# Kernel tuning notes

Measured on AMD Instinct MI355X. Metric: run time of the kernel, lower is better.

The kernel has to match this reference:

```python
import jax, jax.numpy as jnp
import numpy as np

DIM = 1024          # hidden_size
MOE_HID = 512       # moe_intermediate_size
SHARED_HID = 2048   # shared_expert_intermediate_size
N_EXPERTS = 16
TOP_K = 2
NORM_TOPK_PROB = True


def setup_inputs() -> dict:
    key = jax.random.key(0)
    ks = jax.random.split(key, 9)
    s = 0.02  # init scale
    x = jax.random.normal(ks[0], (2, 1024, DIM), dtype=jnp.float32)
    Wg = jax.random.normal(ks[1], (N_EXPERTS, DIM), dtype=jnp.float32) * s
    We_gate = jax.random.normal(ks[2], (N_EXPERTS, MOE_HID, DIM), dtype=jnp.float32) * s
    We_up = jax.random.normal(ks[3], (N_EXPERTS, MOE_HID, DIM), dtype=jnp.float32) * s
    We_down = jax.random.normal(ks[4], (N_EXPERTS, DIM, MOE_HID), dtype=jnp.float32) * s
    Ws_gate = jax.random.normal(ks[5], (SHARED_HID, DIM), dtype=jnp.float32) * s
    Ws_up = jax.random.normal(ks[6], (SHARED_HID, DIM), dtype=jnp.float32) * s
    Ws_down = jax.random.normal(ks[7], (DIM, SHARED_HID), dtype=jnp.float32) * s
    Wsg = jax.random.normal(ks[8], (1, DIM), dtype=jnp.float32) * s
    return {"x": x, "Wg": Wg, "We_gate": We_gate, "We_up": We_up,
            "We_down": We_down, "Ws_gate": Ws_gate, "Ws_up": Ws_up,
            "Ws_down": Ws_down, "Wsg": Wsg}


def reference(x, Wg, We_gate, We_up, We_down, Ws_gate, Ws_up, Ws_down, Wsg):
    B, S, D = x.shape
    xt = x.reshape(-1, D)  # [T, D] tokens
    # router: softmax over experts, then top-k
    gates = jax.nn.softmax(xt @ Wg.T, axis=-1)          # [T, E]
    scores, inds = jax.lax.top_k(gates, TOP_K)           # [T, K]
    if NORM_TOPK_PROB:
        scores = scores / jnp.sum(scores, axis=-1, keepdims=True)
    # experts: SwiGLU computed for all experts, then gather the top-k outputs
    g = jnp.einsum('td,ehd->teh', xt, We_gate)           # [T, E, H]
    u = jnp.einsum('td,ehd->teh', xt, We_up)             # [T, E, H]
    h = jax.nn.silu(g) * u                               # swiglu
    y_all = jnp.einsum('teh,edh->ted', h, We_down)       # [T, E, D]
    y_sel = jnp.take_along_axis(y_all, inds[:, :, None], axis=1)  # [T, K, D]
    y = jnp.sum(y_sel * scores[:, :, None], axis=1)      # [T, D]
    # shared expert with sigmoid gate
    shared = (jax.nn.silu(xt @ Ws_gate.T) * (xt @ Ws_up.T)) @ Ws_down.T  # [T, D]
    y = y + jax.nn.sigmoid(xt @ Wsg.T) * shared
    return y.reshape(B, S, D)
```

## Files before the change

kernel.cpp:

```cpp
#include <hip/hip_runtime.h>
#include <stdint.h>

#define DIM 1024
#define MOE_HID 512
#define SH_HID 2048
#define NE 16
#define NT 2048
#define ROWS_CAP 6144

typedef unsigned short u16;
typedef __attribute__((ext_vector_type(8))) short s16x8;
typedef __attribute__((ext_vector_type(4))) float f32x4;

#define SYNC_BAR() \
  asm volatile("s_waitcnt lgkmcnt(0)" ::: "memory"); \
  __builtin_amdgcn_sched_barrier(0); \
  __builtin_amdgcn_s_barrier(); \
  __builtin_amdgcn_sched_barrier(0);

__device__ __forceinline__ u16 f2bf(float f){
  union { float f; unsigned v; } x; x.f = f;
  unsigned r = x.v + 0x7FFF + ((x.v >> 16) & 1);
  return (u16)(r >> 16);
}

__device__ __forceinline__ s16x8 cvt8pk(float4 a, float4 b){
  union { s16x8 v; unsigned u[4]; } r;
  asm volatile("v_cvt_pk_bf16_f32 %0, %1, %2" : "=v"(r.u[0]) : "v"(a.x), "v"(a.y));
  asm volatile("v_cvt_pk_bf16_f32 %0, %1, %2" : "=v"(r.u[1]) : "v"(a.z), "v"(a.w));
  asm volatile("v_cvt_pk_bf16_f32 %0, %1, %2" : "=v"(r.u[2]) : "v"(b.x), "v"(b.y));
  asm volatile("v_cvt_pk_bf16_f32 %0, %1, %2" : "=v"(r.u[3]) : "v"(b.z), "v"(b.w));
  return r.v;
}

__global__ void k_cvt_x(const float* __restrict__ s, u16* __restrict__ d){
  int i = (blockIdx.x * 256 + threadIdx.x) * 4;
  float4 v = *(const float4*)(s + i);
  ushort4 o;
  o.x = f2bf(v.x); o.y = f2bf(v.y); o.z = f2bf(v.z); o.w = f2bf(v.w);
  *(ushort4*)(d + i) = o;
}

__global__ void k_router(const float* __restrict__ x, const float* __restrict__ Wg,
                         const float* __restrict__ Wsgate1,
                         int* __restrict__ inds, float* __restrict__ scores,
                         float* __restrict__ gl){
  int lane = threadIdx.x & 63;
  int t = blockIdx.x * 4 + (threadIdx.x >> 6);
  const float4* xt = (const float4*)(x + (size_t)t * DIM);
  float4 xv[4];
#pragma unroll
  for(int j = 0; j < 4; j++) xv[j] = xt[lane + 64 * j];

  float acc[NE + 1];
#pragma unroll
  for(int e = 0; e <= NE; e++) acc[e] = 0.f;

#pragma unroll
  for(int e = 0; e < NE; e++){
    const float4* wr = (const float4*)(Wg + (size_t)e * DIM);
#pragma unroll
    for(int j = 0; j < 4; j++){
      float4 w = wr[lane + 64 * j];
      acc[e] += xv[j].x * w.x + xv[j].y * w.y + xv[j].z * w.z + xv[j].w * w.w;
    }
  }
  {
    const float4* wr = (const float4*)Wsgate1;
#pragma unroll
    for(int j = 0; j < 4; j++){
      float4 w = wr[lane + 64 * j];
      acc[NE] += xv[j].x * w.x + xv[j].y * w.y + xv[j].z * w.z + xv[j].w * w.w;
    }
  }

#pragma unroll
  for(int off = 32; off; off >>= 1)
#pragma unroll
    for(int e = 0; e <= NE; e++) acc[e] += __shfl_xor(acc[e], off, 64);

  if(lane == 0){
    int b0 = 0; float v0 = acc[0];
    for(int e = 1; e < NE; e++) if(acc[e] > v0){ v0 = acc[e]; b0 = e; }
    int b1 = (b0 == 0) ? 1 : 0; float v1 = acc[b1];
    for(int e = 0; e < NE; e++) if(e != b0 && acc[e] > v1){ v1 = acc[e]; b1 = e; }
    float s0 = 1.f / (1.f + __expf(v1 - v0));
    inds[t*2+0] = b0; inds[t*2+1] = b1;
    scores[t*2+0] = s0; scores[t*2+1] = 1.f - s0;
    gl[t] = acc[NE];
  }
}

__global__ void k_assign(const int* __restrict__ inds, const float* __restrict__ scores,
                         int* __restrict__ counts, int* __restrict__ offs,
                         int* __restrict__ rowinfo, float* __restrict__ rowscore){
  __shared__ int cnt[NE], off_s[NE], fill[NE];
  int tid = threadIdx.x;
  if(tid < NE){ cnt[tid] = 0; fill[tid] = 0; }
  __syncthreads();
  int ea[4];
#pragma unroll
  for(int i = 0; i < 4; i++){
    int a = tid + 1024 * i;
    ea[i] = inds[a];
    atomicAdd(&cnt[ea[i]], 1);
  }
  __syncthreads();
  if(tid == 0){
    int o = 0;
    for(int e = 0; e < NE; e++){
      off_s[e] = o;
      o += (cnt[e] + 127) & ~127;
    }
  }
  __syncthreads();
#pragma unroll
  for(int i = 0; i < 4; i++){
    int a = tid + 1024 * i;
    int e = ea[i];
    int row = off_s[e] + atomicAdd(&fill[e], 1);
    rowinfo[row] = a;
    rowscore[row] = scores[a];
  }
  if(tid < NE){ counts[tid] = cnt[tid]; offs[tid] = off_s[tid]; }
}

__global__ __launch_bounds__(256, 2) void k_gateup_fused(
    const u16* __restrict__ xb, const int* __restrict__ rowinfo,
    const float* __restrict__ Weg, const float* __restrict__ Weu,
    const float* __restrict__ Wsg, const float* __restrict__ Wsu,
    u16* __restrict__ Hm, u16* __restrict__ Hs,
    const int* __restrict__ counts, const int* __restrict__ offs){
  __shared__ __align__(16) u16 As[2][128 * 64];
  __shared__ __align__(16) u16 Bgs[2][64 * 64];
  __shared__ __align__(16) u16 Bus[2][64 * 64];

  const int bid = blockIdx.x;
  const int tid = threadIdx.x, lane = tid & 63, wid = tid >> 6;
  const int wm = wid >> 1, wn = wid & 1;
  const int srow = tid >> 2;
  const int p16 = (tid & 3) * 16;
  const int cb = (tid & 3) * 2;
  const int key = srow & 7;
  const int fr = lane & 15;
  const int fc = lane >> 4;
  const int fx = fr & 7;

  const int wA00 = (srow     ) * 64 + ((cb    ) ^ key) * 8;
  const int wA01 = (srow     ) * 64 + ((cb + 1) ^ key) * 8;
  const int wA10 = (srow + 64) * 64 + ((cb    ) ^ key) * 8;
  const int wA11 = (srow + 64) * 64 + ((cb + 1) ^ key) * 8;
  const int wB0  = srow * 64 + ((cb    ) ^ key) * 8;
  const int wB1  = srow * 64 + ((cb + 1) ^ key) * 8;

  const u16 *Ar0, *Ar1;
  const float *Bgr, *Bur;
  u16* H; int ldh;

  if(bid < 384){
    const int row0 = (bid >> 3) * 128;
    const int n0 = (bid & 7) * 64;
    const int rows_used = offs[NE-1] + ((counts[NE-1] + 127) & ~127);
    if(row0 >= rows_used) return;
    int e = 0;
#pragma unroll
    for(int k = 1; k < NE; k++) if(row0 >= offs[k]) e = k;

    int a0 = rowinfo[row0 + srow];
    int a1 = rowinfo[row0 + 64 + srow];
    int t0 = ((unsigned)a0 < 4096u) ? (a0 >> 1) : 0;
    int t1 = ((unsigned)a1 < 4096u) ? (a1 >> 1) : 0;
    Ar0 = xb + (size_t)t0 * DIM + p16;
    Ar1 = xb + (size_t)t1 * DIM + p16;
    Bgr = Weg + (size_t)e * MOE_HID * DIM + (size_t)((bid & 7) * 64 + srow) * DIM + p16;
    Bur = Weu + (size_t)e * MOE_HID * DIM + (size_t)((bid & 7) * 64 + srow) * DIM + p16;
    H = Hm + (size_t)row0 * MOE_HID + n0;
    ldh = MOE_HID;
  } else {
    const int i = bid - 384;
    const int row0 = (i >> 5) * 128;
    const int n0 = (i & 31) * 64;
    Ar0 = xb + (size_t)(row0 + srow) * DIM + p16;
    Ar1 = xb + (size_t)(row0 + 64 + srow) * DIM + p16;
    Bgr = Wsg + (size_t)(n0 + srow) * DIM + p16;
    Bur = Wsu + (size_t)(n0 + srow) * DIM + p16;
    H = Hs + (size_t)row0 * SH_HID + n0;
    ldh = SH_HID;
  }

  uint4 aE00, aE01, aE10, aE11, aO00, aO01, aO10, aO11;
  float4 gE0, gE1, gE2, gE3, uE0, uE1, uE2, uE3;
  float4 gO0, gO1, gO2, gO3, uO0, uO1, uO2, uO3;

#define GF_LOAD(S, ko) \
  a##S##00 = *(const uint4*)(Ar0 + (ko));      a##S##01 = *(const uint4*)(Ar0 + (ko) + 8); \
  a##S##10 = *(const uint4*)(Ar1 + (ko));      a##S##11 = *(const uint4*)(Ar1 + (ko) + 8); \
  g##S##0 = *(const float4*)(Bgr + (ko));      g##S##1 = *(const float4*)(Bgr + (ko) + 4); \
  g##S##2 = *(const float4*)(Bgr + (ko) + 8);  g##S##3 = *(const float4*)(Bgr + (ko) + 12); \
  u##S##0 = *(const float4*)(Bur + (ko));      u##S##1 = *(const float4*)(Bur + (ko) + 4); \
  u##S##2 = *(const float4*)(Bur + (ko) + 8);  u##S##3 = *(const float4*)(Bur + (ko) + 12);

  f32x4 accg[4][2], accu[4][2];
#pragma unroll
  for(int m = 0; m < 4; m++)
#pragma unroll
    for(int n = 0; n < 2; n++){
      accg[m][n] = (f32x4){0.f,0.f,0.f,0.f};
      accu[m][n] = (f32x4){0.f,0.f,0.f,0.f};
    }

  GF_LOAD(E, 0)
  GF_LOAD(O, 64)

#define GF_STEP(tt, S, bb) { \
  *(uint4*)(As[bb] + wA00) = a##S##00; \
  *(uint4*)(As[bb] + wA01) = a##S##01; \
  *(uint4*)(As[bb] + wA10) = a##S##10; \
  *(uint4*)(As[bb] + wA11) = a##S##11; \
  *(s16x8*)(Bgs[bb] + wB0) = cvt8pk(g##S##0, g##S##1); \
  *(s16x8*)(Bgs[bb] + wB1) = cvt8pk(g##S##2, g##S##3); \
  *(s16x8*)(Bus[bb] + wB0) = cvt8pk(u##S##0, u##S##1); \
  *(s16x8*)(Bus[bb] + wB1) = cvt8pk(u##S##2, u##S##3); \
  SYNC_BAR() \
  if((tt) + 2 < 16){ GF_LOAD(S, ((tt) + 2) * 64) } \
  s16x8 af[4][2], bgf[2][2], buf2[2][2]; \
  _Pragma("unroll") for(int m = 0; m < 4; m++){ \
    int r = wm*64 + m*16 + fr; \
    _Pragma("unroll") for(int ks = 0; ks < 2; ks++) \
      af[m][ks] = *(const s16x8*)(As[bb] + r*64 + (((ks*4 + fc) ^ fx)) * 8); } \
  _Pragma("unroll") for(int n = 0; n < 2; n++){ \
    int r = wn*32 + n*16 + fr; \
    _Pragma("unroll") for(int ks = 0; ks < 2; ks++){ \
      bgf[n][ks]  = *(const s16x8*)(Bgs[bb] + r*64 + (((ks*4 + fc) ^ fx)) * 8); \
      buf2[n][ks] = *(const s16x8*)(Bus[bb] + r*64 + (((ks*4 + fc) ^ fx)) * 8); } } \
  _Pragma("unroll") for(int m = 0; m < 4; m++) \
  _Pragma("unroll") for(int n = 0; n < 2; n++){ \
    accg[m][n] = __builtin_amdgcn_mfma_f32_16x16x32_bf16(af[m][0], bgf[n][0], accg[m][n], 0, 0, 0); \
    accg[m][n] = __builtin_amdgcn_mfma_f32_16x16x32_bf16(af[m][1], bgf[n][1], accg[m][n], 0, 0, 0); \
    accu[m][n] = __builtin_amdgcn_mfma_f32_16x16x32_bf16(af[m][0], buf2[n][0], accu[m][n], 0, 0, 0); \
    accu[m][n] = __builtin_amdgcn_mfma_f32_16x16x32_bf16(af[m][1], buf2[n][1], accu[m][n], 0, 0, 0); } }

  for(int t = 0; t < 16; t += 2){
    GF_STEP(t,     E, 0)
    GF_STEP(t + 1, O, 1)
  }

#pragma unroll
  for(int m = 0; m < 4; m++)
#pragma unroll
    for(int n = 0; n < 2; n++)
#pragma unroll
      for(int i = 0; i < 4; i++){
        int r = wm*64 + m*16 + ((lane >> 4) << 2) + i;
        int c = wn*32 + n*16 + (lane & 15);
        float g = accg[m][n][i], u = accu[m][n][i];
        float h = (g / (1.f + __expf(-g))) * u;
        H[(size_t)r * ldh + c] = f2bf(h);
      }
}

__global__ __launch_bounds__(256, 2) void k_down_all(
    const u16* __restrict__ Hm, const u16* __restrict__ Hs,
    const float* __restrict__ Wed, const float* __restrict__ Wsd,
    float* __restrict__ yp, float* __restrict__ Sh0, float* __restrict__ Sh1,
    const int* __restrict__ counts, const int* __restrict__ offs,
    const int* __restrict__ rowinfo, const float* __restrict__ rowscore){
  __shared__ __align__(16) u16 As[2][128 * 32];
  __shared__ __align__(16) u16 Bs[2][128 * 32];

  const int y = blockIdx.y, n0 = blockIdx.x * 128;
  const bool sh = (y < 32);
  const u16* A; const float* B; float* O = yp;
  int lda, M = NT, row0 = 0, kBeg = 0, nk, lrow = 0;
  if(sh){
    int mtile = y & 15, kz = y >> 4;
    A = Hs + (size_t)mtile * 128 * SH_HID; lda = SH_HID;
    B = Wsd; kBeg = kz * 1024; nk = 32;
    O = (kz == 0) ? Sh0 : Sh1;
    row0 = mtile * 128;
  } else {
    row0 = (y - 32) * 128;
    int rows_used = offs[NE-1] + ((counts[NE-1] + 127) & ~127);
    if(row0 >= rows_used) return;
    int e = 0;
#pragma unroll
    for(int k = 1; k < NE; k++) if(row0 >= offs[k]) e = k;
    M = counts[e];
    lrow = row0 - offs[e];
    A = Hm + (size_t)row0 * MOE_HID; lda = MOE_HID;
    B = Wed + (size_t)e * DIM * MOE_HID; nk = 16;
  }

  const int tid = threadIdx.x, lane = tid & 63, wid = tid >> 6;
  const int wm = wid >> 1, wn = wid & 1;
  const int srow = tid >> 2, p8 = (tid & 3) * 8;
  const int swz8 = (((tid & 3) ^ ((tid >> 3) & 3))) * 8;
  const int fr = lane & 15;
  const int fkswz = (((lane >> 4) ^ ((lane >> 1) & 3))) * 8;
  const int wA0 = srow * 32 + swz8, wA1 = (64 + srow) * 32 + swz8;

  const u16* Ar0 = A + (size_t)srow * lda + kBeg + p8;
  const u16* Ar1 = A + (size_t)(64 + srow) * lda + kBeg + p8;
  const float* Br0 = B + (size_t)(n0 + srow) * lda + kBeg + p8;
  const float* Br1 = B + (size_t)(n0 + 64 + srow) * lda + kBeg + p8;

  uint4 aE0, aE1, aO0, aO1;
  float4 bE00, bE01, bE10, bE11, bO00, bO01, bO10, bO11;

#define DN_LOAD(S, ko) \
  a##S##0 = *(const uint4*)(Ar0 + (ko));   a##S##1 = *(const uint4*)(Ar1 + (ko)); \
  b##S##00 = *(const float4*)(Br0 + (ko)); b##S##01 = *(const float4*)(Br0 + (ko) + 4); \
  b##S##10 = *(const float4*)(Br1 + (ko)); b##S##11 = *(const float4*)(Br1 + (ko) + 4);

  f32x4 acc[4][4];
#pragma unroll
  for(int m = 0; m < 4; m++)
#pragma unroll
    for(int n = 0; n < 4; n++) acc[m][n] = (f32x4){0.f,0.f,0.f,0.f};

  DN_LOAD(E, 0)
  DN_LOAD(O, 32)

#define DN_STEP(tt, S, bb) { \
  *(uint4*)(As[bb] + wA0) = a##S##0; \
  *(uint4*)(As[bb] + wA1) = a##S##1; \
  *(s16x8*)(Bs[bb] + wA0) = cvt8pk(b##S##00, b##S##01); \
  *(s16x8*)(Bs[bb] + wA1) = cvt8pk(b##S##10, b##S##11); \
  SYNC_BAR() \
  if((tt) + 2 < nk){ DN_LOAD(S, ((tt) + 2) * 32) } \
  s16x8 af[4], bf[4]; \
  _Pragma("unroll") for(int m = 0; m < 4; m++) \
    af[m] = *(const s16x8*)(As[bb] + (wm*64 + m*16 + fr) * 32 + fkswz); \
  _Pragma("unroll") for(int n = 0; n < 4; n++) \
    bf[n] = *(const s16x8*)(Bs[bb] + (wn*64 + n*16 + fr) * 32 + fkswz); \
  _Pragma("unroll") for(int m = 0; m < 4; m++) \
  _Pragma("unroll") for(int n = 0; n < 4; n++) \
    acc[m][n] = __builtin_amdgcn_mfma_f32_16x16x32_bf16(af[m], bf[n], acc[m][n], 0, 0, 0); }

  for(int t = 0; t < nk; t += 2){
    DN_STEP(t,     E, 0)
    DN_STEP(t + 1, O, 1)
  }

#pragma unroll
  for(int m = 0; m < 4; m++)
#pragma unroll
    for(int i = 0; i < 4; i++){
      int rl = wm*64 + m*16 + ((lane >> 4) << 2) + i;
      if(sh){
        float* orow = O + (size_t)(row0 + rl) * DIM + n0 + wn*64 + (lane & 15);
#pragma unroll
        for(int n = 0; n < 4; n++) orow[n*16] = acc[m][n][i];
      } else if(lrow + rl < M){
        int ar = row0 + rl;
        int slot = rowinfo[ar];
        float sc = rowscore[ar];
        float* orow = yp + (size_t)slot * DIM + n0 + wn*64 + (lane & 15);
#pragma unroll
        for(int n = 0; n < 4; n++) orow[n*16] = sc * acc[m][n][i];
      }
    }
}

__global__ void k_combine(const float* __restrict__ yp, const float* __restrict__ Sh0,
                          const float* __restrict__ Sh1,
                          const float* __restrict__ gl, float* __restrict__ out){
  int idx = (blockIdx.x * 256 + threadIdx.x) * 4;
  int t = idx >> 10;
  float s = 1.f / (1.f + __expf(-gl[t]));
  float4 a = *(const float4*)(yp + (size_t)(t*2)   * DIM + (idx & 1023));
  float4 b = *(const float4*)(yp + (size_t)(t*2+1) * DIM + (idx & 1023));
  float4 c0 = *(const float4*)(Sh0 + idx);
  float4 c1 = *(const float4*)(Sh1 + idx);
  float4 o;
  o.x = a.x + b.x + s * (c0.x + c1.x);
  o.y = a.y + b.y + s * (c0.y + c1.y);
  o.z = a.z + b.z + s * (c0.z + c1.z);
  o.w = a.w + b.w + s * (c0.w + c1.w);
  *(float4*)(out + idx) = o;
}

extern "C" void kernel_launch(void* const* d_in, const int* in_sizes, int n_in,
                              void* d_out, int out_size, void* d_ws, size_t ws_size,
                              hipStream_t stream){
  const float* x    = (const float*)d_in[0];
  const float* Wg   = (const float*)d_in[1];
  const float* Weg  = (const float*)d_in[2];
  const float* Weu  = (const float*)d_in[3];
  const float* Wed  = (const float*)d_in[4];
  const float* Wsg  = (const float*)d_in[5];
  const float* Wsu  = (const float*)d_in[6];
  const float* Wsd  = (const float*)d_in[7];
  const float* Wg1  = (const float*)d_in[8];
  float* out = (float*)d_out;

  char* p = (char*)d_ws;
  int* inds   = (int*)p;  p += 4096 * 4;
  float* scores = (float*)p; p += 4096 * 4;
  float* gl   = (float*)p;  p += NT * 4;
  int* counts = (int*)p;  p += 64;
  int* offs   = (int*)p;  p += 64;
  int* rowinfo = (int*)p; p += ROWS_CAP * 4;
  float* rowscore = (float*)p; p += ROWS_CAP * 4;
  u16* xb     = (u16*)p;  p += (size_t)NT * DIM * 2;
  u16* Hs     = (u16*)p;  p += (size_t)NT * SH_HID * 2;
  float* Sh0  = (float*)p; p += (size_t)NT * DIM * 4;
  float* Sh1  = (float*)p; p += (size_t)NT * DIM * 4;
  u16* Hm     = (u16*)p;  p += (size_t)ROWS_CAP * MOE_HID * 2;
  float* yp   = (float*)p; p += (size_t)NT * 2 * DIM * 4;

  k_router<<<NT/4, 256, 0, stream>>>(x, Wg, Wg1, inds, scores, gl);
  k_cvt_x<<<NT * DIM / (256 * 4), 256, 0, stream>>>(x, xb);
  k_assign<<<1, 1024, 0, stream>>>(inds, scores, counts, offs, rowinfo, rowscore);

  k_gateup_fused<<<896, 256, 0, stream>>>(xb, rowinfo, Weg, Weu, Wsg, Wsu,
                                          Hm, Hs, counts, offs);
  k_down_all<<<dim3(8, 80), 256, 0, stream>>>(Hm, Hs, Wed, Wsd,
                                              yp, Sh0, Sh1, counts, offs,
                                              rowinfo, rowscore);

  k_combine<<<2048, 256, 0, stream>>>(yp, Sh0, Sh1, gl, out);
}
```

Before: 115.6 us.

## Fuse x bf16 conversion into router and combine via atomic adds in down kernel

The fp32-to-bf16 conversion of x moves into the router kernel, which already loads x, so one launch and one extra read of x go away. The separate combine kernel and its intermediate buffers (yp, Sh0, Sh1) are removed. The down-projection kernel now scales by the sigmoid shared gate or the routing score and atomically adds straight into a zero-initialised output. This drops several large fp32 intermediate writes and reads, at the cost of a memset, fp32 atomic traffic, and a summation order that is no longer deterministic.

```diff
diff --git a/kernel.cpp b/kernel.cpp
--- a/kernel.cpp
+++ b/kernel.cpp
@@ -33,24 +33,23 @@
   return r.v;
 }
 
-__global__ void k_cvt_x(const float* __restrict__ s, u16* __restrict__ d){
-  int i = (blockIdx.x * 256 + threadIdx.x) * 4;
-  float4 v = *(const float4*)(s + i);
-  ushort4 o;
-  o.x = f2bf(v.x); o.y = f2bf(v.y); o.z = f2bf(v.z); o.w = f2bf(v.w);
-  *(ushort4*)(d + i) = o;
-}
-
 __global__ void k_router(const float* __restrict__ x, const float* __restrict__ Wg,
                          const float* __restrict__ Wsgate1,
                          int* __restrict__ inds, float* __restrict__ scores,
-                         float* __restrict__ gl){
+                         float* __restrict__ gl, u16* __restrict__ xb){
   int lane = threadIdx.x & 63;
   int t = blockIdx.x * 4 + (threadIdx.x >> 6);
   const float4* xt = (const float4*)(x + (size_t)t * DIM);
   float4 xv[4];
 #pragma unroll
   for(int j = 0; j < 4; j++) xv[j] = xt[lane + 64 * j];
+
+#pragma unroll
+  for(int j = 0; j < 4; j++){
+    ushort4 o;
+    o.x = f2bf(xv[j].x); o.y = f2bf(xv[j].y); o.z = f2bf(xv[j].z); o.w = f2bf(xv[j].w);
+    *(ushort4*)(xb + (size_t)t * DIM + 4 * (lane + 64 * j)) = o;
+  }
 
   float acc[NE + 1];
 #pragma unroll
@@ -262,7 +261,7 @@
 __global__ __launch_bounds__(256, 2) void k_down_all(
     const u16* __restrict__ Hm, const u16* __restrict__ Hs,
     const float* __restrict__ Wed, const float* __restrict__ Wsd,
-    float* __restrict__ yp, float* __restrict__ Sh0, float* __restrict__ Sh1,
+    float* __restrict__ out, const float* __restrict__ gl,
     const int* __restrict__ counts, const int* __restrict__ offs,
     const int* __restrict__ rowinfo, const float* __restrict__ rowscore){
   __shared__ __align__(16) u16 As[2][128 * 32];
@@ -270,13 +269,12 @@
 
   const int y = blockIdx.y, n0 = blockIdx.x * 128;
   const bool sh = (y < 32);
-  const u16* A; const float* B; float* O = yp;
+  const u16* A; const float* B;
   int lda, M = NT, row0 = 0, kBeg = 0, nk, lrow = 0;
   if(sh){
     int mtile = y & 15, kz = y >> 4;
     A = Hs + (size_t)mtile * 128 * SH_HID; lda = SH_HID;
     B = Wsd; kBeg = kz * 1024; nk = 32;
-    O = (kz == 0) ? Sh0 : Sh1;
     row0 = mtile * 128;
   } else {
     row0 = (y - 32) * 128;
@@ -348,36 +346,21 @@
     for(int i = 0; i < 4; i++){
       int rl = wm*64 + m*16 + ((lane >> 4) << 2) + i;
       if(sh){
-        float* orow = O + (size_t)(row0 + rl) * DIM + n0 + wn*64 + (lane & 15);
-#pragma unroll
-        for(int n = 0; n < 4; n++) orow[n*16] = acc[m][n][i];
+        int token = row0 + rl;
+        float s = 1.f / (1.f + __expf(-gl[token]));
+        float* orow = out + (size_t)token * DIM + n0 + wn*64 + (lane & 15);
+#pragma unroll
+        for(int n = 0; n < 4; n++) atomicAdd(&orow[n*16], s * acc[m][n][i]);
       } else if(lrow + rl < M){
         int ar = row0 + rl;
         int slot = rowinfo[ar];
         float sc = rowscore[ar];
-        float* orow = yp + (size_t)slot * DIM + n0 + wn*64 + (lane & 15);
-#pragma unroll
-        for(int n = 0; n < 4; n++) orow[n*16] = sc * acc[m][n][i];
+        int token = slot >> 1;
+        float* orow = out + (size_t)token * DIM + n0 + wn*64 + (lane & 15);
+#pragma unroll
+        for(int n = 0; n < 4; n++) atomicAdd(&orow[n*16], sc * acc[m][n][i]);
       }
     }
-}
-
-__global__ void k_combine(const float* __restrict__ yp, const float* __restrict__ Sh0,
-                          const float* __restrict__ Sh1,
-                          const float* __restrict__ gl, float* __restrict__ out){
-  int idx = (blockIdx.x * 256 + threadIdx.x) * 4;
-  int t = idx >> 10;
-  float s = 1.f / (1.f + __expf(-gl[t]));
-  float4 a = *(const float4*)(yp + (size_t)(t*2)   * DIM + (idx & 1023));
-  float4 b = *(const float4*)(yp + (size_t)(t*2+1) * DIM + (idx & 1023));
-  float4 c0 = *(const float4*)(Sh0 + idx);
-  float4 c1 = *(const float4*)(Sh1 + idx);
-  float4 o;
-  o.x = a.x + b.x + s * (c0.x + c1.x);
-  o.y = a.y + b.y + s * (c0.y + c1.y);
-  o.z = a.z + b.z + s * (c0.z + c1.z);
-  o.w = a.w + b.w + s * (c0.w + c1.w);
-  *(float4*)(out + idx) = o;
 }
 
 extern "C" void kernel_launch(void* const* d_in, const int* in_sizes, int n_in,
@@ -404,20 +387,16 @@
   float* rowscore = (float*)p; p += ROWS_CAP * 4;
   u16* xb     = (u16*)p;  p += (size_t)NT * DIM * 2;
   u16* Hs     = (u16*)p;  p += (size_t)NT * SH_HID * 2;
-  float* Sh0  = (float*)p; p += (size_t)NT * DIM * 4;
-  float* Sh1  = (float*)p; p += (size_t)NT * DIM * 4;
   u16* Hm     = (u16*)p;  p += (size_t)ROWS_CAP * MOE_HID * 2;
-  float* yp   = (float*)p; p += (size_t)NT * 2 * DIM * 4;
-
-  k_router<<<NT/4, 256, 0, stream>>>(x, Wg, Wg1, inds, scores, gl);
-  k_cvt_x<<<NT * DIM / (256 * 4), 256, 0, stream>>>(x, xb);
+
+  hipMemsetAsync(out, 0, (size_t)out_size * 4, stream);
+
+  k_router<<<NT/4, 256, 0, stream>>>(x, Wg, Wg1, inds, scores, gl, xb);
   k_assign<<<1, 1024, 0, stream>>>(inds, scores, counts, offs, rowinfo, rowscore);
 
   k_gateup_fused<<<896, 256, 0, stream>>>(xb, rowinfo, Weg, Weu, Wsg, Wsu,
                                           Hm, Hs, counts, offs);
   k_down_all<<<dim3(8, 80), 256, 0, stream>>>(Hm, Hs, Wed, Wsd,
-                                              yp, Sh0, Sh1, counts, offs,
+                                              out, gl, counts, offs,
                                               rowinfo, rowscore);
-
-  k_combine<<<2048, 256, 0, stream>>>(yp, Sh0, Sh1, gl, out);
-}
+}
```

Measured after the change: 125.7 us. 8.8% more time.
